# Optimization experiments

Hardware: AMD Instinct MI355X
Metric: run time of the kernel (lower is better)

Reference implementation:

```python
import jax, jax.numpy as jnp
import numpy as np

L, H, D, DH, FF, CTX, S, V = 12, 12, 768, 64, 3072, 1536, 8, 1024
B, T = 2, 1024


def setup_inputs() -> dict:
    key = jax.random.key(0)
    ks = jax.random.split(key, 12)
    init = lambda k, shape, fan_in: jax.random.normal(k, shape, jnp.float32) * (fan_in ** -0.5)
    return {
        "prev_tokens": jax.random.randint(ks[0], (B, T, S), 0, V),
        "positions": jnp.tile(jnp.arange(T, dtype=jnp.int32), (B, 1)),
        "intent_vec": jax.random.normal(ks[1], (B, 1, D), jnp.float32) * 0.02,
        "rvq_embed": jax.random.normal(ks[2], (S, V, D), jnp.float32) * 0.02,
        "pos_embed": jax.random.normal(ks[3], (CTX, D), jnp.float32) * 0.02,
        "norm1_w": jnp.ones((L, D), jnp.float32),
        "norm2_w": jnp.ones((L, D), jnp.float32),
        "qkv_w": init(ks[4], (L, 3 * D, D), D),
        "proj_w": init(ks[5], (L, D, D), D),
        "gate_w": init(ks[6], (L, FF, D), D),
        "up_w": init(ks[7], (L, FF, D), D),
        "down_w": init(ks[8], (L, D, FF), FF),
        "normf_w": jnp.ones((D,), jnp.float32),
        "heads_w": init(ks[9], (S, V, D), D),
    }


def _rmsnorm(x, w, eps=1e-6):
    return x * jax.lax.rsqrt(jnp.mean(x * x, axis=-1, keepdims=True) + eps) * w


def reference(prev_tokens, positions, intent_vec, rvq_embed, pos_embed,
              norm1_w, norm2_w, qkv_w, proj_w, gate_w, up_w, down_w,
              normf_w, heads_w):
    # 8-way RVQ embedding sum + positional + intent  -> [B, T, D]
    stage_idx = jnp.arange(S)[None, None, :]               # [1,1,S]
    x = rvq_embed[stage_idx, prev_tokens].sum(axis=2)      # gather [B,T,S,D] -> sum
    x = x + pos_embed[positions] + intent_vec

    scale = DH ** -0.5
    mask = jnp.tril(jnp.ones((T, T), dtype=bool))          # causal (prefill path)

    for l in range(L):
        # attention block (pre-norm)
        h = _rmsnorm(x, norm1_w[l])
        qkv = jnp.einsum('btd,ed->bte', h, qkv_w[l]).reshape(B, T, 3, H, DH)
        q = jnp.moveaxis(qkv[:, :, 0], 1, 2)               # [B,H,T,DH]
        k = jnp.moveaxis(qkv[:, :, 1], 1, 2)
        v = jnp.moveaxis(qkv[:, :, 2], 1, 2)
        att = jnp.einsum('bhqd,bhkd->bhqk', q, k) * scale
        att = jnp.where(mask, att, -jnp.inf)
        att = jax.nn.softmax(att, axis=-1)
        o = jnp.einsum('bhqk,bhkd->bhqd', att, v)
        o = jnp.moveaxis(o, 1, 2).reshape(B, T, D)
        x = x + jnp.einsum('btd,ed->bte', o, proj_w[l])
        # SwiGLU FFN block
        h = _rmsnorm(x, norm2_w[l])
        g = jax.nn.silu(jnp.einsum('btd,fd->btf', h, gate_w[l]))
        u = jnp.einsum('btd,fd->btf', h, up_w[l])
        x = x + jnp.einsum('btf,df->btd', g * u, down_w[l])

    x = _rmsnorm(x, normf_w)
    last = x[:, -1, :]                                     # [B, D]
    logits = jnp.einsum('bd,svd->sbv', last, heads_w)      # per-stage logits [S,B,V]
    return logits
```

## Files before the change

### kernel.cpp

```cpp
#include <hip/hip_runtime.h>
#include <hip/hip_bf16.h>

#define LAYERS 12
#define NH     12
#define D      768
#define DH     64
#define FF     3072
#define NS     8
#define NV     1024
#define BB     2
#define TT     1024
#define BT     (BB*TT)

typedef __attribute__((ext_vector_type(8))) short  short8;
typedef __attribute__((ext_vector_type(8))) unsigned short ushort8;
typedef __attribute__((ext_vector_type(4))) float  floatx4;

#define PITCH 72

__device__ __forceinline__ float wave_sum(float v) {
    v += __shfl_xor(v, 1);  v += __shfl_xor(v, 2);  v += __shfl_xor(v, 4);
    v += __shfl_xor(v, 8);  v += __shfl_xor(v, 16); v += __shfl_xor(v, 32);
    return v;
}
__device__ __forceinline__ unsigned short f2bf(float f) {
    unsigned int u = __builtin_bit_cast(unsigned int, f);
    u += 0x7fffu + ((u >> 16) & 1u);
    return (unsigned short)(u >> 16);
}
__device__ __forceinline__ ushort8 pack8(float4 f0, float4 f1) {
    ushort8 r;
    r[0]=f2bf(f0.x); r[1]=f2bf(f0.y); r[2]=f2bf(f0.z); r[3]=f2bf(f0.w);
    r[4]=f2bf(f1.x); r[5]=f2bf(f1.y); r[6]=f2bf(f1.z); r[7]=f2bf(f1.w);
    return r;
}

__global__ __launch_bounds__(256) void embed_kernel(
    const int* __restrict__ prev_tokens, const int* __restrict__ positions,
    const float* __restrict__ intent, const float* __restrict__ rvq,
    const float* __restrict__ pos_emb, float* __restrict__ x) {
    const int row = blockIdx.x;
    const int b   = row >> 10;
    __shared__ int toks[NS];
    __shared__ int p;
    if (threadIdx.x < NS) toks[threadIdx.x] = prev_tokens[row * NS + threadIdx.x];
    if (threadIdx.x == NS) p = positions[row];
    __syncthreads();
    for (int d = threadIdx.x; d < D; d += 256) {
        float acc = intent[b * D + d] + pos_emb[p * D + d];
        #pragma unroll
        for (int s = 0; s < NS; ++s)
            acc += rvq[((size_t)(s * NV + toks[s])) * D + d];
        x[(size_t)row * D + d] = acc;
    }
}

__global__ __launch_bounds__(256) void rmsnorm_kernel(
    const float* __restrict__ x, const float* __restrict__ w, unsigned short* __restrict__ h) {
    const int row = blockIdx.x;
    const float* xr = x + (size_t)row * D;
    float ss = 0.f;
    for (int d = threadIdx.x; d < D; d += 256) { float v = xr[d]; ss += v * v; }
    const int wave = threadIdx.x >> 6, lane = threadIdx.x & 63;
    __shared__ float red[4];
    float s = wave_sum(ss);
    if (lane == 0) red[wave] = s;
    __syncthreads();
    float tot = red[0] + red[1] + red[2] + red[3];
    float inv = rsqrtf(tot * (1.0f / D) + 1e-6f);
    for (int d = threadIdx.x; d < D; d += 256)
        h[(size_t)row * D + d] = f2bf(xr[d] * inv * w[d]);
}

template <int MODE, int SPLITK>
__global__ __launch_bounds__(256) void gemm128(
    const unsigned short* __restrict__ A, const float* __restrict__ W,
    void* __restrict__ Cv, int M, int N, int K) {
    __shared__ unsigned short As[128 * PITCH];
    __shared__ unsigned short Ws[128 * PITCH];
    const int tid  = threadIdx.x;
    const int row0 = blockIdx.y * 128;
    const int col0 = blockIdx.x * 128;
    const int kchunk = K / SPLITK;
    const int kbeg = blockIdx.z * kchunk;
    const int kend = kbeg + kchunk;
    const int wv = tid >> 6, lane = tid & 63;
    const int l15 = lane & 15, quad = lane >> 4;
    const int wm = (wv & 1) * 64, wn = (wv >> 1) * 64;

    floatx4 acc[4][4];
    #pragma unroll
    for (int i = 0; i < 4; ++i)
        #pragma unroll
        for (int j = 0; j < 4; ++j) acc[i][j] = (floatx4){0.f, 0.f, 0.f, 0.f};

    for (int k0 = kbeg; k0 < kend; k0 += 64) {
        ushort8 a_ld[4], w_ld[4];
        #pragma unroll
        for (int q = 0; q < 4; ++q) {
            const int ch = tid + 256 * q;
            const int r = ch >> 3, sl = ch & 7;
            a_ld[q] = *(const ushort8*)(A + (size_t)(row0 + r) * K + k0 + sl * 8);
            const float* wp = W + (size_t)(col0 + r) * K + k0 + sl * 8;
            float4 f0 = *(const float4*)(wp);
            float4 f1 = *(const float4*)(wp + 4);
            w_ld[q] = pack8(f0, f1);
        }
        __syncthreads();
        #pragma unroll
        for (int q = 0; q < 4; ++q) {
            const int ch = tid + 256 * q;
            const int r = ch >> 3, sl = ch & 7;
            *(ushort8*)(&As[r * PITCH + sl * 8]) = a_ld[q];
            *(ushort8*)(&Ws[r * PITCH + sl * 8]) = w_ld[q];
        }
        __syncthreads();
        #pragma unroll
        for (int ks = 0; ks < 2; ++ks) {
            short8 af[4], bf[4];
            #pragma unroll
            for (int i = 0; i < 4; ++i)
                af[i] = *(const short8*)(&As[(wm + i * 16 + l15) * PITCH + ks * 32 + quad * 8]);
            #pragma unroll
            for (int j = 0; j < 4; ++j)
                bf[j] = *(const short8*)(&Ws[(wn + j * 16 + l15) * PITCH + ks * 32 + quad * 8]);
            #pragma unroll
            for (int i = 0; i < 4; ++i)
                #pragma unroll
                for (int j = 0; j < 4; ++j)
                    acc[i][j] = __builtin_amdgcn_mfma_f32_16x16x32_bf16(af[i], bf[j], acc[i][j], 0, 0, 0);
        }
    }

    #pragma unroll
    for (int i = 0; i < 4; ++i) {
        #pragma unroll
        for (int j = 0; j < 4; ++j) {
            const int n = col0 + wn + j * 16 + l15;
            #pragma unroll
            for (int r = 0; r < 4; ++r) {
                const int m = row0 + wm + i * 16 + quad * 4 + r;
                const float v = acc[i][j][r];
                if (MODE == 2) {
                    ((float*)Cv)[(size_t)m * N + n] += v;
                } else if (MODE == 3) {
                    atomicAdd(&((float*)Cv)[(size_t)m * N + n], v);
                } else {
                    const int wsel = n / D;
                    const int rr = n - wsel * D;
                    const int hh = rr >> 6, dd = rr & 63;
                    const int b = m >> 10, t = m & 1023;
                    ((unsigned short*)Cv)[(size_t)wsel * (BT * D) +
                        (((size_t)(b * NH + hh)) * TT + t) * DH + dd] =
                        f2bf(wsel == 0 ? v * 0.125f : v);
                }
            }
        }
    }
}

__global__ __launch_bounds__(256) void gateup128(
    const unsigned short* __restrict__ A, const float* __restrict__ Wg,
    const float* __restrict__ Wu, unsigned short* __restrict__ gbf, int K) {
    __shared__ unsigned short As[128 * PITCH];
    __shared__ unsigned short Gs[64 * PITCH];
    __shared__ unsigned short Us[64 * PITCH];
    const int tid  = threadIdx.x;
    const int row0 = blockIdx.y * 128;
    const int col0 = blockIdx.x * 64;
    const int wv = tid >> 6, lane = tid & 63;
    const int l15 = lane & 15, quad = lane >> 4;
    const int wm = (wv & 1) * 64, wn = (wv >> 1) * 32;

    floatx4 ag[4][2], au[4][2];
    #pragma unroll
    for (int i = 0; i < 4; ++i)
        #pragma unroll
        for (int j = 0; j < 2; ++j) {
            ag[i][j] = (floatx4){0.f, 0.f, 0.f, 0.f};
            au[i][j] = (floatx4){0.f, 0.f, 0.f, 0.f};
        }

    for (int k0 = 0; k0 < K; k0 += 64) {
        ushort8 a_ld[4], w_ld[4];
        #pragma unroll
        for (int q = 0; q < 4; ++q) {
            const int ch = tid + 256 * q;
            const int r = ch >> 3, sl = ch & 7;
            a_ld[q] = *(const ushort8*)(A + (size_t)(row0 + r) * K + k0 + sl * 8);
            const int p  = (ch & 511);
            const int wr = p >> 3, wsl = p & 7;
            const float* wp = (q < 2 ? Wg : Wu) + (size_t)(col0 + wr) * K + k0 + wsl * 8;
            float4 f0 = *(const float4*)(wp);
            float4 f1 = *(const float4*)(wp + 4);
            w_ld[q] = pack8(f0, f1);
        }
        __syncthreads();
        #pragma unroll
        for (int q = 0; q < 4; ++q) {
            const int ch = tid + 256 * q;
            const int r = ch >> 3, sl = ch & 7;
            *(ushort8*)(&As[r * PITCH + sl * 8]) = a_ld[q];
            const int p  = (ch & 511);
            const int wr = p >> 3, wsl = p & 7;
            unsigned short* dst = (q < 2 ? Gs : Us);
            *(ushort8*)(&dst[wr * PITCH + wsl * 8]) = w_ld[q];
        }
        __syncthreads();
        #pragma unroll
        for (int ks = 0; ks < 2; ++ks) {
            short8 af[4], bg[2], bu[2];
            #pragma unroll
            for (int i = 0; i < 4; ++i)
                af[i] = *(const short8*)(&As[(wm + i * 16 + l15) * PITCH + ks * 32 + quad * 8]);
            #pragma unroll
            for (int j = 0; j < 2; ++j) {
                bg[j] = *(const short8*)(&Gs[(wn + j * 16 + l15) * PITCH + ks * 32 + quad * 8]);
                bu[j] = *(const short8*)(&Us[(wn + j * 16 + l15) * PITCH + ks * 32 + quad * 8]);
            }
            #pragma unroll
            for (int i = 0; i < 4; ++i)
                #pragma unroll
                for (int j = 0; j < 2; ++j) {
                    ag[i][j] = __builtin_amdgcn_mfma_f32_16x16x32_bf16(af[i], bg[j], ag[i][j], 0, 0, 0);
                    au[i][j] = __builtin_amdgcn_mfma_f32_16x16x32_bf16(af[i], bu[j], au[i][j], 0, 0, 0);
                }
        }
    }

    #pragma unroll
    for (int i = 0; i < 4; ++i) {
        #pragma unroll
        for (int j = 0; j < 2; ++j) {
            const int n = col0 + wn + j * 16 + l15;
            #pragma unroll
            for (int r = 0; r < 4; ++r) {
                const int m = row0 + wm + i * 16 + quad * 4 + r;
                const float gv = ag[i][j][r], uv = au[i][j][r];
                gbf[(size_t)m * FF + n] = f2bf(gv / (1.f + __expf(-gv)) * uv);
            }
        }
    }
}

#define KP 72
__global__ __launch_bounds__(256) void attn_mfma(
    const unsigned short* __restrict__ qkv, unsigned short* __restrict__ obf) {
    const int bh = blockIdx.y;
    const int b = bh / NH, h = bh - b * NH;
    const int qt = blockIdx.x;
    const int q0 = qt * 64;
    const int tid = threadIdx.x;
    const int wv = tid >> 6, lane = tid & 63;
    const int l15 = lane & 15, quad = lane >> 4;

    const unsigned short* Q = qkv + (size_t)bh * TT * DH;
    const unsigned short* K = qkv + (size_t)BT * D + (size_t)bh * TT * DH;
    const unsigned short* V = qkv + 2 * (size_t)BT * D + (size_t)bh * TT * DH;

    __shared__ unsigned short Ks[64 * KP];
    __shared__ unsigned short Vts[64 * KP];
    __shared__ unsigned short Pa[64 * KP];

    short8 qf[2];
    #pragma unroll
    for (int c = 0; c < 2; ++c)
        qf[c] = *(const short8*)(Q + (size_t)(q0 + wv * 16 + l15) * DH + c * 32 + quad * 8);

    floatx4 o_acc[4];
    #pragma unroll
    for (int j = 0; j < 4; ++j) o_acc[j] = (floatx4){0.f, 0.f, 0.f, 0.f};
    float m_run[4] = {-INFINITY, -INFINITY, -INFINITY, -INFINITY};
    float l_run[4] = {0.f, 0.f, 0.f, 0.f};

    for (int kt = 0; kt <= qt; ++kt) {
        __syncthreads();
        {
            const int krow = tid >> 2, kq = tid & 3;
            const unsigned short* kg = K + (size_t)(kt * 64 + krow) * DH + kq * 16;
            ushort8 k0v = *(const ushort8*)(kg);
            ushort8 k1v = *(const ushort8*)(kg + 8);
            *(ushort8*)(&Ks[krow * KP + kq * 16])     = k0v;
            *(ushort8*)(&Ks[krow * KP + kq * 16 + 8]) = k1v;
            const int kp = tid & 31, chunk = tid >> 5;
            const unsigned short* vg = V + (size_t)(kt * 64 + 2 * kp) * DH + chunk * 8;
            ushort8 v0 = *(const ushort8*)(vg);
            ushort8 v1 = *(const ushort8*)(vg + DH);
            #pragma unroll
            for (int j = 0; j < 8; ++j) {
                unsigned int pk = (unsigned int)v0[j] | ((unsigned int)v1[j] << 16);
                *(unsigned int*)(&Vts[(chunk * 8 + j) * KP + 2 * kp]) = pk;
            }
        }
        __syncthreads();

        floatx4 s[4];
        #pragma unroll
        for (int j = 0; j < 4; ++j) {
            short8 kb0 = *(const short8*)(&Ks[(j * 16 + l15) * KP + quad * 8]);
            short8 kb1 = *(const short8*)(&Ks[(j * 16 + l15) * KP + 32 + quad * 8]);
            floatx4 z = (floatx4){0.f, 0.f, 0.f, 0.f};
            z = __builtin_amdgcn_mfma_f32_16x16x32_bf16(qf[0], kb0, z, 0, 0, 0);
            s[j] = __builtin_amdgcn_mfma_f32_16x16x32_bf16(qf[1], kb1, z, 0, 0, 0);
        }
        if (kt == qt) {
            #pragma unroll
            for (int j = 0; j < 4; ++j) {
                const int k_rel = j * 16 + l15;
                #pragma unroll
                for (int r = 0; r < 4; ++r) {
                    const int q_rel = wv * 16 + quad * 4 + r;
                    if (k_rel > q_rel) s[j][r] = -INFINITY;
                }
            }
        }
        #pragma unroll
        for (int r = 0; r < 4; ++r) {
            float mt = fmaxf(fmaxf(s[0][r], s[1][r]), fmaxf(s[2][r], s[3][r]));
            mt = fmaxf(mt, __shfl_xor(mt, 1));
            mt = fmaxf(mt, __shfl_xor(mt, 2));
            mt = fmaxf(mt, __shfl_xor(mt, 4));
            mt = fmaxf(mt, __shfl_xor(mt, 8));
            const float m_new = fmaxf(m_run[r], mt);
            const float alpha = __expf(m_run[r] - m_new);
            float rs = 0.f;
            #pragma unroll
            for (int j = 0; j < 4; ++j) {
                const float p = __expf(s[j][r] - m_new);
                s[j][r] = p;
                rs += p;
            }
            rs += __shfl_xor(rs, 1);
            rs += __shfl_xor(rs, 2);
            rs += __shfl_xor(rs, 4);
            rs += __shfl_xor(rs, 8);
            l_run[r] = l_run[r] * alpha + rs;
            m_run[r] = m_new;
            #pragma unroll
            for (int j = 0; j < 4; ++j) o_acc[j][r] *= alpha;
        }
        #pragma unroll
        for (int j = 0; j < 4; ++j)
            #pragma unroll
            for (int r = 0; r < 4; ++r)
                Pa[(wv * 16 + quad * 4 + r) * KP + j * 16 + l15] = f2bf(s[j][r]);
        short8 pa0 = *(const short8*)(&Pa[(wv * 16 + l15) * KP + quad * 8]);
        short8 pa1 = *(const short8*)(&Pa[(wv * 16 + l15) * KP + 32 + quad * 8]);
        #pragma unroll
        for (int j = 0; j < 4; ++j) {
            short8 vb0 = *(const short8*)(&Vts[(j * 16 + l15) * KP + quad * 8]);
            short8 vb1 = *(const short8*)(&Vts[(j * 16 + l15) * KP + 32 + quad * 8]);
            o_acc[j] = __builtin_amdgcn_mfma_f32_16x16x32_bf16(pa0, vb0, o_acc[j], 0, 0, 0);
            o_acc[j] = __builtin_amdgcn_mfma_f32_16x16x32_bf16(pa1, vb1, o_acc[j], 0, 0, 0);
        }
    }
    #pragma unroll
    for (int j = 0; j < 4; ++j) {
        #pragma unroll
        for (int r = 0; r < 4; ++r) {
            const int t = q0 + wv * 16 + quad * 4 + r;
            const int ch = h * DH + j * 16 + l15;
            obf[((size_t)(b * TT + t)) * D + ch] = f2bf(o_acc[j][r] / l_run[r]);
        }
    }
}

__global__ __launch_bounds__(256) void final_norm_kernel(
    const float* __restrict__ x, const float* __restrict__ w, float* __restrict__ last) {
    const int b = blockIdx.x;
    const float* xr = x + ((size_t)(b * TT + (TT - 1))) * D;
    float ss = 0.f;
    for (int d = threadIdx.x; d < D; d += 256) { float v = xr[d]; ss += v * v; }
    const int wave = threadIdx.x >> 6, lane = threadIdx.x & 63;
    __shared__ float red[4];
    float s = wave_sum(ss);
    if (lane == 0) red[wave] = s;
    __syncthreads();
    float tot = red[0] + red[1] + red[2] + red[3];
    float inv = rsqrtf(tot * (1.0f / D) + 1e-6f);
    for (int d = threadIdx.x; d < D; d += 256)
        last[(size_t)b * D + d] = xr[d] * inv * w[d];
}

__global__ __launch_bounds__(256) void heads_kernel(
    const float* __restrict__ last, const float* __restrict__ hw, float* __restrict__ out) {
    const int gw = (blockIdx.x * 256 + threadIdx.x) >> 6;
    const int lane = threadIdx.x & 63;
    const int s = gw >> 10, v = gw & 1023;
    const float* w = hw + (size_t)gw * D;
    float a0 = 0.f, a1 = 0.f;
    for (int d = lane; d < D; d += 64) {
        const float ww = w[d];
        a0 = fmaf(ww, last[d], a0);
        a1 = fmaf(ww, last[D + d], a1);
    }
    a0 = wave_sum(a0);
    a1 = wave_sum(a1);
    if (lane == 0) {
        out[((size_t)s * BB + 0) * NV + v] = a0;
        out[((size_t)s * BB + 1) * NV + v] = a1;
    }
}

extern "C" void kernel_launch(void* const* d_in, const int* in_sizes, int n_in,
                              void* d_out, int out_size, void* d_ws, size_t ws_size,
                              hipStream_t stream) {
    const int*   prev_tokens = (const int*)  d_in[0];
    const int*   positions   = (const int*)  d_in[1];
    const float* intent      = (const float*)d_in[2];
    const float* rvq         = (const float*)d_in[3];
    const float* pos_emb     = (const float*)d_in[4];
    const float* norm1_w     = (const float*)d_in[5];
    const float* norm2_w     = (const float*)d_in[6];
    const float* qkv_w       = (const float*)d_in[7];
    const float* proj_w      = (const float*)d_in[8];
    const float* gate_w      = (const float*)d_in[9];
    const float* up_w        = (const float*)d_in[10];
    const float* down_w      = (const float*)d_in[11];
    const float* normf_w     = (const float*)d_in[12];
    const float* heads_w     = (const float*)d_in[13];
    float* out = (float*)d_out;

    char* base = (char*)d_ws;
    float* x   = (float*)base;                       base += (size_t)BT * D * 4;
    float* last= (float*)base;                       base += 2 * D * 4;
    unsigned short* hbf    = (unsigned short*)base;  base += (size_t)BT * D * 2;
    unsigned short* qkvbf  = (unsigned short*)base;  base += (size_t)3 * BT * D * 2;
    unsigned short* obf    = (unsigned short*)base;  base += (size_t)BT * D * 2;
    unsigned short* gbf    = (unsigned short*)base;  base += (size_t)BT * FF * 2;

    embed_kernel<<<BT, 256, 0, stream>>>(prev_tokens, positions, intent, rvq, pos_emb, x);

    for (int l = 0; l < LAYERS; ++l) {
        rmsnorm_kernel<<<BT, 256, 0, stream>>>(x, norm1_w + l * D, hbf);
        gemm128<1, 1><<<dim3(3 * D / 128, BT / 128, 1), 256, 0, stream>>>(
            hbf, qkv_w + (size_t)l * 3 * D * D, qkvbf, BT, 3 * D, D);
        attn_mfma<<<dim3(TT / 64, BB * NH), 256, 0, stream>>>(qkvbf, obf);
        gemm128<3, 2><<<dim3(D / 128, BT / 128, 2), 256, 0, stream>>>(
            obf, proj_w + (size_t)l * D * D, x, BT, D, D);
        rmsnorm_kernel<<<BT, 256, 0, stream>>>(x, norm2_w + l * D, hbf);
        gateup128<<<dim3(FF / 64, BT / 128), 256, 0, stream>>>(
            hbf, gate_w + (size_t)l * FF * D, up_w + (size_t)l * FF * D, gbf, D);
        gemm128<3, 4><<<dim3(D / 128, BT / 128, 4), 256, 0, stream>>>(
            gbf, down_w + (size_t)l * D * FF, x, BT, D, FF);
    }

    final_norm_kernel<<<2, 256, 0, stream>>>(x, normf_w, last);
    heads_kernel<<<(NS * NV * 64) / 256, 256, 0, stream>>>(last, heads_w, out);
}
```

Baseline: 2.521 ms.

## Pre-convert weights to bf16 and stage GEMM tiles via direct global-to-LDS loads

After: 2.218 ms. -12.0%, faster.

```diff
diff --git a/kernel.cpp b/kernel.cpp
--- a/kernel.cpp
+++ b/kernel.cpp
@@ -16,8 +16,6 @@
 typedef __attribute__((ext_vector_type(8))) unsigned short ushort8;
 typedef __attribute__((ext_vector_type(4))) float  floatx4;
 
-#define PITCH 72
-
 __device__ __forceinline__ float wave_sum(float v) {
     v += __shfl_xor(v, 1);  v += __shfl_xor(v, 2);  v += __shfl_xor(v, 4);
     v += __shfl_xor(v, 8);  v += __shfl_xor(v, 16); v += __shfl_xor(v, 32);
@@ -33,6 +31,22 @@
     r[0]=f2bf(f0.x); r[1]=f2bf(f0.y); r[2]=f2bf(f0.z); r[3]=f2bf(f0.w);
     r[4]=f2bf(f1.x); r[5]=f2bf(f1.y); r[6]=f2bf(f1.z); r[7]=f2bf(f1.w);
     return r;
+}
+__device__ __forceinline__ void gl2lds16(const void* g, void* l) {
+    __builtin_amdgcn_global_load_lds(
+        (const __attribute__((address_space(1))) unsigned int*)g,
+        (__attribute__((address_space(3))) unsigned int*)l, 16, 0, 0);
+}
+
+__global__ __launch_bounds__(256) void cvt_bf16_kernel(
+    const float* __restrict__ w, unsigned short* __restrict__ o, int n8) {
+    const int i = blockIdx.x * 256 + threadIdx.x;
+    if (i < n8) {
+        const float* p = w + (size_t)i * 8;
+        float4 f0 = *(const float4*)p;
+        float4 f1 = *(const float4*)(p + 4);
+        *(ushort8*)(o + (size_t)i * 8) = pack8(f0, f1);
+    }
 }
 
 __global__ __launch_bounds__(256) void embed_kernel(
@@ -74,10 +88,10 @@
 
 template <int MODE, int SPLITK>
 __global__ __launch_bounds__(256) void gemm128(
-    const unsigned short* __restrict__ A, const float* __restrict__ W,
+    const unsigned short* __restrict__ A, const unsigned short* __restrict__ W,
     void* __restrict__ Cv, int M, int N, int K) {
-    __shared__ unsigned short As[128 * PITCH];
-    __shared__ unsigned short Ws[128 * PITCH];
+    __shared__ unsigned short As[128 * 64];
+    __shared__ unsigned short Ws[128 * 64];
     const int tid  = threadIdx.x;
     const int row0 = blockIdx.y * 128;
     const int col0 = blockIdx.x * 128;
@@ -87,6 +101,8 @@
     const int wv = tid >> 6, lane = tid & 63;
     const int l15 = lane & 15, quad = lane >> 4;
     const int wm = (wv & 1) * 64, wn = (wv >> 1) * 64;
+    const int rb = tid >> 3;
+    const int sl = tid & 7;
 
     floatx4 acc[4][4];
     #pragma unroll
@@ -95,35 +111,30 @@
         for (int j = 0; j < 4; ++j) acc[i][j] = (floatx4){0.f, 0.f, 0.f, 0.f};
 
     for (int k0 = kbeg; k0 < kend; k0 += 64) {
-        ushort8 a_ld[4], w_ld[4];
+        __syncthreads();
         #pragma unroll
         for (int q = 0; q < 4; ++q) {
-            const int ch = tid + 256 * q;
-            const int r = ch >> 3, sl = ch & 7;
-            a_ld[q] = *(const ushort8*)(A + (size_t)(row0 + r) * K + k0 + sl * 8);
-            const float* wp = W + (size_t)(col0 + r) * K + k0 + sl * 8;
-            float4 f0 = *(const float4*)(wp);
-            float4 f1 = *(const float4*)(wp + 4);
-            w_ld[q] = pack8(f0, f1);
-        }
-        __syncthreads();
-        #pragma unroll
-        for (int q = 0; q < 4; ++q) {
-            const int ch = tid + 256 * q;
-            const int r = ch >> 3, sl = ch & 7;
-            *(ushort8*)(&As[r * PITCH + sl * 8]) = a_ld[q];
-            *(ushort8*)(&Ws[r * PITCH + sl * 8]) = w_ld[q];
+            const int r = q * 32 + rb;
+            const int gsl = sl ^ (r & 7);
+            gl2lds16(A + (size_t)(row0 + r) * K + k0 + gsl * 8,
+                     &As[(q * 256 + wv * 64) * 8]);
+            gl2lds16(W + (size_t)(col0 + r) * K + k0 + gsl * 8,
+                     &Ws[(q * 256 + wv * 64) * 8]);
         }
         __syncthreads();
         #pragma unroll
         for (int ks = 0; ks < 2; ++ks) {
             short8 af[4], bf[4];
             #pragma unroll
-            for (int i = 0; i < 4; ++i)
-                af[i] = *(const short8*)(&As[(wm + i * 16 + l15) * PITCH + ks * 32 + quad * 8]);
-            #pragma unroll
-            for (int j = 0; j < 4; ++j)
-                bf[j] = *(const short8*)(&Ws[(wn + j * 16 + l15) * PITCH + ks * 32 + quad * 8]);
+            for (int i = 0; i < 4; ++i) {
+                const int r = wm + i * 16 + l15;
+                af[i] = *(const short8*)(&As[r * 64 + (((ks * 4 + quad) ^ (r & 7)) * 8)]);
+            }
+            #pragma unroll
+            for (int j = 0; j < 4; ++j) {
+                const int r = wn + j * 16 + l15;
+                bf[j] = *(const short8*)(&Ws[r * 64 + (((ks * 4 + quad) ^ (r & 7)) * 8)]);
+            }
             #pragma unroll
             for (int i = 0; i < 4; ++i)
                 #pragma unroll
@@ -141,9 +152,7 @@
             for (int r = 0; r < 4; ++r) {
                 const int m = row0 + wm + i * 16 + quad * 4 + r;
                 const float v = acc[i][j][r];
-                if (MODE == 2) {
-                    ((float*)Cv)[(size_t)m * N + n] += v;
-                } else if (MODE == 3) {
+                if (MODE == 3) {
                     atomicAdd(&((float*)Cv)[(size_t)m * N + n], v);
                 } else {
                     const int wsel = n / D;
@@ -160,17 +169,19 @@
 }
 
 __global__ __launch_bounds__(256) void gateup128(
-    const unsigned short* __restrict__ A, const float* __restrict__ Wg,
-    const float* __restrict__ Wu, unsigned short* __restrict__ gbf, int K) {
-    __shared__ unsigned short As[128 * PITCH];
-    __shared__ unsigned short Gs[64 * PITCH];
-    __shared__ unsigned short Us[64 * PITCH];
+    const unsigned short* __restrict__ A, const unsigned short* __restrict__ Wg,
+    const unsigned short* __restrict__ Wu, unsigned short* __restrict__ gbf, int K) {
+    __shared__ unsigned short As[128 * 64];
+    __shared__ unsigned short Gs[64 * 64];
+    __shared__ unsigned short Us[64 * 64];
     const int tid  = threadIdx.x;
     const int row0 = blockIdx.y * 128;
     const int col0 = blockIdx.x * 64;
     const int wv = tid >> 6, lane = tid & 63;
     const int l15 = lane & 15, quad = lane >> 4;
     const int wm = (wv & 1) * 64, wn = (wv >> 1) * 32;
+    const int rb = tid >> 3;
+    const int sl = tid & 7;
 
     floatx4 ag[4][2], au[4][2];
     #pragma unroll
@@ -182,41 +193,40 @@
         }
 
     for (int k0 = 0; k0 < K; k0 += 64) {
-        ushort8 a_ld[4], w_ld[4];
+        __syncthreads();
         #pragma unroll
         for (int q = 0; q < 4; ++q) {
-            const int ch = tid + 256 * q;
-            const int r = ch >> 3, sl = ch & 7;
-            a_ld[q] = *(const ushort8*)(A + (size_t)(row0 + r) * K + k0 + sl * 8);
-            const int p  = (ch & 511);
-            const int wr = p >> 3, wsl = p & 7;
-            const float* wp = (q < 2 ? Wg : Wu) + (size_t)(col0 + wr) * K + k0 + wsl * 8;
-            float4 f0 = *(const float4*)(wp);
-            float4 f1 = *(const float4*)(wp + 4);
-            w_ld[q] = pack8(f0, f1);
-        }
-        __syncthreads();
-        #pragma unroll
-        for (int q = 0; q < 4; ++q) {
-            const int ch = tid + 256 * q;
-            const int r = ch >> 3, sl = ch & 7;
-            *(ushort8*)(&As[r * PITCH + sl * 8]) = a_ld[q];
-            const int p  = (ch & 511);
-            const int wr = p >> 3, wsl = p & 7;
-            unsigned short* dst = (q < 2 ? Gs : Us);
-            *(ushort8*)(&dst[wr * PITCH + wsl * 8]) = w_ld[q];
+            const int r = q * 32 + rb;
+            const int gsl = sl ^ (r & 7);
+            gl2lds16(A + (size_t)(row0 + r) * K + k0 + gsl * 8,
+                     &As[(q * 256 + wv * 64) * 8]);
+        }
+        {
+            #pragma unroll
+            for (int q = 0; q < 2; ++q) {
+                const int r = q * 32 + rb;
+                const int gsl = sl ^ (r & 7);
+                gl2lds16(Wg + (size_t)(col0 + r) * K + k0 + gsl * 8,
+                         &Gs[(q * 256 + wv * 64) * 8]);
+                gl2lds16(Wu + (size_t)(col0 + r) * K + k0 + gsl * 8,
+                         &Us[(q * 256 + wv * 64) * 8]);
+            }
         }
         __syncthreads();
         #pragma unroll
         for (int ks = 0; ks < 2; ++ks) {
             short8 af[4], bg[2], bu[2];
             #pragma unroll
-            for (int i = 0; i < 4; ++i)
-                af[i] = *(const short8*)(&As[(wm + i * 16 + l15) * PITCH + ks * 32 + quad * 8]);
+            for (int i = 0; i < 4; ++i) {
+                const int r = wm + i * 16 + l15;
+                af[i] = *(const short8*)(&As[r * 64 + (((ks * 4 + quad) ^ (r & 7)) * 8)]);
+            }
             #pragma unroll
             for (int j = 0; j < 2; ++j) {
-                bg[j] = *(const short8*)(&Gs[(wn + j * 16 + l15) * PITCH + ks * 32 + quad * 8]);
-                bu[j] = *(const short8*)(&Us[(wn + j * 16 + l15) * PITCH + ks * 32 + quad * 8]);
+                const int r = wn + j * 16 + l15;
+                const int off = r * 64 + (((ks * 4 + quad) ^ (r & 7)) * 8);
+                bg[j] = *(const short8*)(&Gs[off]);
+                bu[j] = *(const short8*)(&Us[off]);
             }
             #pragma unroll
             for (int i = 0; i < 4; ++i)
@@ -423,26 +433,42 @@
 
     char* base = (char*)d_ws;
     float* x   = (float*)base;                       base += (size_t)BT * D * 4;
-    float* last= (float*)base;                       base += 2 * D * 4;
+    float* last= (float*)base;                       base += 4096;
     unsigned short* hbf    = (unsigned short*)base;  base += (size_t)BT * D * 2;
     unsigned short* qkvbf  = (unsigned short*)base;  base += (size_t)3 * BT * D * 2;
     unsigned short* obf    = (unsigned short*)base;  base += (size_t)BT * D * 2;
     unsigned short* gbf    = (unsigned short*)base;  base += (size_t)BT * FF * 2;
+    unsigned short* wqkv = (unsigned short*)base;    base += (size_t)LAYERS * 3 * D * D * 2;
+    unsigned short* wproj= (unsigned short*)base;    base += (size_t)LAYERS * D * D * 2;
+    unsigned short* wgate= (unsigned short*)base;    base += (size_t)LAYERS * FF * D * 2;
+    unsigned short* wup  = (unsigned short*)base;    base += (size_t)LAYERS * FF * D * 2;
+    unsigned short* wdown= (unsigned short*)base;    base += (size_t)LAYERS * D * FF * 2;
+
+    {
+        const int n_qkv  = LAYERS * 3 * D * D / 8;
+        const int n_proj = LAYERS * D * D / 8;
+        const int n_ff   = LAYERS * FF * D / 8;
+        cvt_bf16_kernel<<<(n_qkv  + 255) / 256, 256, 0, stream>>>(qkv_w,  wqkv,  n_qkv);
+        cvt_bf16_kernel<<<(n_proj + 255) / 256, 256, 0, stream>>>(proj_w, wproj, n_proj);
+        cvt_bf16_kernel<<<(n_ff   + 255) / 256, 256, 0, stream>>>(gate_w, wgate, n_ff);
+        cvt_bf16_kernel<<<(n_ff   + 255) / 256, 256, 0, stream>>>(up_w,   wup,   n_ff);
+        cvt_bf16_kernel<<<(n_ff   + 255) / 256, 256, 0, stream>>>(down_w, wdown, n_ff);
+    }
 
     embed_kernel<<<BT, 256, 0, stream>>>(prev_tokens, positions, intent, rvq, pos_emb, x);
 
     for (int l = 0; l < LAYERS; ++l) {
         rmsnorm_kernel<<<BT, 256, 0, stream>>>(x, norm1_w + l * D, hbf);
         gemm128<1, 1><<<dim3(3 * D / 128, BT / 128, 1), 256, 0, stream>>>(
-            hbf, qkv_w + (size_t)l * 3 * D * D, qkvbf, BT, 3 * D, D);
+            hbf, wqkv + (size_t)l * 3 * D * D, qkvbf, BT, 3 * D, D);
         attn_mfma<<<dim3(TT / 64, BB * NH), 256, 0, stream>>>(qkvbf, obf);
         gemm128<3, 2><<<dim3(D / 128, BT / 128, 2), 256, 0, stream>>>(
-            obf, proj_w + (size_t)l * D * D, x, BT, D, D);
+            obf, wproj + (size_t)l * D * D, x, BT, D, D);
         rmsnorm_kernel<<<BT, 256, 0, stream>>>(x, norm2_w + l * D, hbf);
         gateup128<<<dim3(FF / 64, BT / 128), 256, 0, stream>>>(
-            hbf, gate_w + (size_t)l * FF * D, up_w + (size_t)l * FF * D, gbf, D);
+            hbf, wgate + (size_t)l * FF * D, wup + (size_t)l * FF * D, gbf, D);
         gemm128<3, 4><<<dim3(D / 128, BT / 128, 4), 256, 0, stream>>>(
-            gbf, down_w + (size_t)l * D * FF, x, BT, D, FF);
+            gbf, wdown + (size_t)l * D * FF, x, BT, D, FF);
     }
 
     final_norm_kernel<<<2, 256, 0, stream>>>(x, normf_w, last);
```
